# Optimization experiments

Hardware: AMD Instinct MI355X
Metric: run time of the kernel (lower is better)

Reference implementation:

```python
import jax, jax.numpy as jnp
import numpy as np
import math

FEAT, HID, EMB, NCLS = 128, 128, 64, 10
N, E = 50000, 1600000
RATIO = 0.8


def graph_conv(x, src, dst, valid, w_rel, b_rel, w_root):
    # PyG GraphConv: out = lin_rel(sum_{j->i} x_j) + lin_root(x_i)
    msg = jnp.where(valid[:, None], x[src], 0.0)  # [E, C]
    seg = jnp.where(valid, dst, x.shape[0])       # invalid -> dummy bucket
    agg = jax.ops.segment_sum(msg, seg, num_segments=x.shape[0] + 1)[:-1]
    return agg @ w_rel.T + b_rel + x @ w_root.T


def topk_pool(x, src, dst, valid, weight):
    # PyG TopKPooling: score = tanh((x . w) / ||w||); keep top ceil(ratio*N)
    score = jnp.tanh((x @ weight) / jnp.linalg.norm(weight))
    k = int(math.ceil(RATIO * x.shape[0]))
    _, perm = jax.lax.top_k(score, k)
    xp = x[perm] * score[perm][:, None]
    mapping = jnp.full((x.shape[0],), -1, dtype=src.dtype)
    mapping = mapping.at[perm].set(jnp.arange(k, dtype=src.dtype))
    nsrc, ndst = mapping[src], mapping[dst]
    nvalid = valid & (nsrc >= 0) & (ndst >= 0)
    return xp, nsrc, ndst, nvalid, perm


def setup_inputs() -> dict:
    key = jax.random.key(0)
    ks = jax.random.split(key, 24)
    s = 0.05
    inp = {
        'x': jax.random.normal(ks[0], (N, FEAT), dtype=jnp.float32),
        'edge_index': jax.random.randint(ks[1], (2, E), 0, N, dtype=jnp.int32),
        'w1_rel': jax.random.normal(ks[2], (HID, FEAT)) * s,
        'w1_root': jax.random.normal(ks[3], (HID, FEAT)) * s,
        'b1': jnp.zeros((HID,), jnp.float32),
        'p1_w': jax.random.normal(ks[4], (HID,)) * s,
        'w2_rel': jax.random.normal(ks[5], (EMB, HID)) * s,
        'w2_root': jax.random.normal(ks[6], (EMB, HID)) * s,
        'b2': jnp.zeros((EMB,), jnp.float32),
        'p2_w': jax.random.normal(ks[7], (EMB,)) * s,
        'w3_rel': jax.random.normal(ks[8], (EMB, EMB)) * s,
        'w3_root': jax.random.normal(ks[9], (EMB, EMB)) * s,
        'b3': jnp.zeros((EMB,), jnp.float32),
        'w4_rel': jax.random.normal(ks[10], (HID, EMB)) * s,
        'w4_root': jax.random.normal(ks[11], (HID, EMB)) * s,
        'b4': jnp.zeros((HID,), jnp.float32),
        'w5_rel': jax.random.normal(ks[12], (FEAT, HID)) * s,
        'w5_root': jax.random.normal(ks[13], (FEAT, HID)) * s,
        'b5': jnp.zeros((FEAT,), jnp.float32),
        'lin_w': jax.random.normal(ks[14], (NCLS, FEAT)) * s,
        'lin_b': jnp.zeros((NCLS,), jnp.float32),
    }
    return inp


def reference(x, edge_index, w1_rel, w1_root, b1, p1_w, w2_rel, w2_root, b2, p2_w,
              w3_rel, w3_root, b3, w4_rel, w4_root, b4, w5_rel, w5_root, b5,
              lin_w, lin_b):
    src0, dst0 = edge_index[0], edge_index[1]
    valid0 = jnp.ones((src0.shape[0],), dtype=bool)

    x1 = jax.nn.relu(graph_conv(x, src0, dst0, valid0, w1_rel, b1, w1_root))
    xp1, src1, dst1, valid1, perm1 = topk_pool(x1, src0, dst0, valid0, p1_w)
    x2 = jax.nn.relu(graph_conv(xp1, src1, dst1, valid1, w2_rel, b2, w2_root))
    xp2, src2, dst2, valid2, perm2 = topk_pool(x2, src1, dst1, valid1, p2_w)
    x3 = jax.nn.relu(graph_conv(xp2, src2, dst2, valid2, w3_rel, b3, w3_root))
    # Unpool1: scatter x3 into zeros shaped like x2, then skip-add
    u1 = jnp.zeros((x2.shape[0], x3.shape[1]), x3.dtype).at[perm2].set(x3) + x2
    x4 = jax.nn.relu(graph_conv(u1, src1, dst1, valid1, w4_rel, b4, w4_root))
    # Unpool2
    u2 = jnp.zeros((x1.shape[0], x4.shape[1]), x4.dtype).at[perm1].set(x4) + x1
    x5 = jax.nn.relu(graph_conv(u2, src0, dst0, valid0, w5_rel, b5, w5_root))
    return jax.nn.log_softmax(x5 @ lin_w.T + lin_b, axis=-1)
```

## Files before the change

### kernel.cpp

```cpp
#include <hip/hip_runtime.h>
#include <hip/hip_bf16.h>
#include <math.h>

#define N0 50000
#define E0 1600000
#define K1 40000
#define K2 32000
#define FEAT 128
#define HID 128
#define EMB 64
#define NCLS 10

#define RADIX_BINS 4096

#define NB 391
#define PB_CH 8192
#define BCAP 5120

#define SCHUNK 2048

typedef __bf16 v8bf __attribute__((ext_vector_type(8)));
typedef __bf16 v4bf __attribute__((ext_vector_type(4)));
typedef float  v4f  __attribute__((ext_vector_type(4)));
typedef unsigned short u16;

static __device__ __forceinline__ unsigned f2key(float f) {
    unsigned u = __float_as_uint(f);
    return (u & 0x80000000u) ? ~u : (u | 0x80000000u);
}

struct SelCtl { unsigned long long prefix; int kRem; int counter; };

__global__ void detect_dtype_kernel(const unsigned* __restrict__ w, int n, int* __restrict__ flag) {
    __shared__ int tot;
    if (threadIdx.x == 0) tot = 0;
    __syncthreads();
    int cnt = 0;
    for (int i = threadIdx.x; i < n; i += 256) {
        unsigned lo = w[i] & 0xFFFFu;
        unsigned e = (lo >> 7) & 0xFFu;
        cnt += (e >= 143);
    }
    atomicAdd(&tot, cnt);
    __syncthreads();
    if (threadIdx.x == 0) flag[0] = (tot > n / 8) ? 1 : 0;
}

static __device__ __forceinline__ float load_as_f32(const void* in, long long i, int isF32) {
    if (isF32) return ((const float*)in)[i];
    unsigned short h = ((const unsigned short*)in)[i];
    return __uint_as_float(((unsigned)h) << 16);
}

__global__ void x_convert_kernel(const void* __restrict__ in, float* __restrict__ xf,
                                 __bf16* __restrict__ hi, __bf16* __restrict__ lo, int n,
                                 const int* __restrict__ flag) {
    int i = blockIdx.x * 256 + threadIdx.x;
    if (i >= n) return;
    float v = load_as_f32(in, i, *flag);
    __bf16 h = (__bf16)v;
    int row = i >> 7, c = i & 127;
    xf[(((size_t)(c >> 4)) * N0 + row) * 16 + (c & 15)] = v;
    hi[i] = h; lo[i] = (__bf16)(v - (float)h);
}

struct SplitJob { const void* src; __bf16* hi; __bf16* lo; int n; };
struct SplitJobs { SplitJob j[10]; };
__global__ void split_all_kernel(SplitJobs jobs, const int* __restrict__ flag) {
    SplitJob jb = jobs.j[blockIdx.y];
    int i = blockIdx.x * 256 + threadIdx.x;
    if (i >= jb.n) return;
    float v = load_as_f32(jb.src, i, *flag);
    __bf16 h = (__bf16)v;
    jb.hi[i] = h; jb.lo[i] = (__bf16)(v - (float)h);
}

struct F32Job { const void* src; float* dst; int n; };
struct F32Jobs { F32Job j[9]; };
__global__ void f32_all_kernel(F32Jobs jobs, const int* __restrict__ flag) {
    F32Job jb = jobs.j[blockIdx.x];
    for (int i = threadIdx.x; i < jb.n; i += 256) jb.dst[i] = load_as_f32(jb.src, i, *flag);
}

template<int KEYS>
__global__ void lookback_scan_kernel(const int* __restrict__ deg,
                                     const unsigned long long* __restrict__ keys,
                                     const SelCtl* __restrict__ ctl, int M,
                                     int* __restrict__ flags,
                                     int* __restrict__ rowp,
                                     int* __restrict__ perm,
                                     int* __restrict__ mapping) {
    int b = blockIdx.x;
    int t = threadIdx.x;
    int lane = t & 63, wave = t >> 6;
    int idx = b * SCHUNK + t * 8;
    unsigned long long thr = KEYS ? ctl->prefix : 0ull;
    int v[8];
#pragma unroll
    for (int k = 0; k < 8; ++k) {
        int j = idx + k;
        if (KEYS) v[k] = (j < M) ? (int)(keys[j] >= thr) : 0;
        else      v[k] = (j < M) ? deg[j] : 0;
    }
    int s = 0;
#pragma unroll
    for (int k = 0; k < 8; ++k) { int tmp = v[k]; v[k] = s; s += tmp; }
    int incl = s;
    for (int off = 1; off < 64; off <<= 1) {
        int u = __shfl_up(incl, off, 64);
        if (lane >= off) incl += u;
    }
    int texcl = incl - s;
    __shared__ int ws[4];
    __shared__ int pfxs;
    if (lane == 63) ws[wave] = incl;
    __syncthreads();
    int woff = 0, T = 0;
    for (int w = 0; w < 4; ++w) { if (w < wave) woff += ws[w]; T += ws[w]; }
    if (t == 0) {
        __threadfence();
        atomicExch(&flags[b], T + 1);
        int sum = 0;
        for (int p = 0; p < b; ++p) {
            int f;
            while ((f = atomicAdd(&flags[p], 0)) == 0) { }
            sum += f - 1;
        }
        pfxs = sum;
    }
    __syncthreads();
    int off0 = pfxs + woff + texcl;
    if (!KEYS) {
#pragma unroll
        for (int k = 0; k < 8; ++k) {
            int j = idx + k;
            if (j < M) rowp[j] = off0 + v[k];
        }
        if (b == gridDim.x - 1 && t == 255) rowp[M] = pfxs + T;
    } else {
#pragma unroll
        for (int k = 0; k < 8; ++k) {
            int j = idx + k;
            if (j < M) {
                if (keys[j] >= thr) { int r = off0 + v[k]; perm[r] = j; mapping[j] = r; }
                else mapping[j] = -1;
            }
        }
    }
}

__global__ void bucket_count_kernel(const int* __restrict__ dst, int E, int* __restrict__ bktCnt) {
    __shared__ int cnt[NB];
    for (int b = threadIdx.x; b < NB; b += 256) cnt[b] = 0;
    __syncthreads();
    int e = blockIdx.x * PB_CH;
    int e1 = E < e + PB_CH ? E : e + PB_CH;
    for (int i = e + threadIdx.x; i < e1; i += 256)
        atomicAdd(&cnt[dst[i] >> 7], 1);
    __syncthreads();
    for (int b = threadIdx.x; b < NB; b += 256) {
        int c = cnt[b];
        if (c) atomicAdd(&bktCnt[b], c);
    }
}

__global__ void scan_nb_kernel(const int* __restrict__ bktCnt, int* __restrict__ bktBase,
                               int* __restrict__ bcur, int* __restrict__ rpM, int E) {
    __shared__ int sc[512];
    int t = threadIdx.x;
    int v = (t < NB) ? bktCnt[t] : 0;
    sc[t] = v;
    __syncthreads();
    for (int off = 1; off < 512; off <<= 1) {
        int u = 0;
        if (t >= off) u = sc[t - off];
        __syncthreads();
        if (t >= off) sc[t] += u;
        __syncthreads();
    }
    if (t < NB) {
        int base = sc[t] - v;
        bktBase[t] = base;
        bcur[t] = base;
    }
    if (t == 0) { bktBase[NB] = E; rpM[0] = E; }
}

__global__ void edge_partition_kernel(const int* __restrict__ src, const int* __restrict__ dst, int E,
                                      int* __restrict__ bcur, unsigned* __restrict__ pairBuf) {
    __shared__ int cnt[NB];
    __shared__ int bas[NB];
    for (int b = threadIdx.x; b < NB; b += 256) cnt[b] = 0;
    __syncthreads();
    int e0 = blockIdx.x * PB_CH;
    int e1 = E < e0 + PB_CH ? E : e0 + PB_CH;
    for (int e = e0 + threadIdx.x; e < e1; e += 256)
        atomicAdd(&cnt[dst[e] >> 7], 1);
    __syncthreads();
    for (int b = threadIdx.x; b < NB; b += 256) {
        int c = cnt[b];
        bas[b] = c ? atomicAdd(&bcur[b], c) : 0;
        cnt[b] = 0;
    }
    __syncthreads();
    for (int e = e0 + threadIdx.x; e < e1; e += 256) {
        int s = src[e];
        int d = dst[e];
        int b = d >> 7;
        int r = atomicAdd(&cnt[b], 1);
        unsigned pv = ((unsigned)(d & 127) << 16) | (unsigned)s;
        __builtin_nontemporal_store(pv, pairBuf + bas[b] + r);
    }
}

__global__ void bucket_fill_kernel(const unsigned* __restrict__ pairBuf, const int* __restrict__ bktBase,
                                   int Mrows, u16* __restrict__ cols, int* __restrict__ rowptr) {
    int b = blockIdx.x;
    int d0 = b << 7;
    int d1 = d0 + 128; if (d1 > Mrows) d1 = Mrows;
    int segBase = bktBase[b], segEnd = bktBase[b + 1];
    int size = segEnd - segBase;
    int tid = threadIdx.x;
    __shared__ int cnt[128];
    __shared__ int sc[128];
    __shared__ int cur[128];
    __shared__ u16 stage[BCAP];
    if (tid < 128) cnt[tid] = 0;
    __syncthreads();
    for (int t = tid; t < size; t += 256)
        atomicAdd(&cnt[pairBuf[segBase + t] >> 16], 1);
    __syncthreads();
    if (tid < 128) sc[tid] = cnt[tid];
    __syncthreads();
    for (int off = 1; off < 128; off <<= 1) {
        int u = 0;
        if (tid < 128 && tid >= off) u = sc[tid - off];
        __syncthreads();
        if (tid < 128 && tid >= off) sc[tid] += u;
        __syncthreads();
    }
    if (tid < 128) {
        int excl = sc[tid] - cnt[tid];
        cur[tid] = excl;
        if (d0 + tid < d1) rowptr[d0 + tid] = segBase + excl;
    }
    __syncthreads();
    if (size <= BCAP) {
        for (int t = tid; t < size; t += 256) {
            unsigned p = pairBuf[segBase + t];
            int pos = atomicAdd(&cur[p >> 16], 1);
            stage[pos] = (u16)(p & 0xFFFFu);
        }
        __syncthreads();
        for (int t = tid; t < size; t += 256)
            __builtin_nontemporal_store(stage[t], cols + segBase + t);
    } else {
        for (int t = tid; t < size; t += 256) {
            unsigned p = pairBuf[segBase + t];
            int pos = atomicAdd(&cur[p >> 16], 1);
            cols[segBase + pos] = (u16)(p & 0xFFFFu);
        }
    }
}

__global__ void deg_filter_kernel(const int* __restrict__ rowptr, const u16* __restrict__ cols,
                                  const int* __restrict__ map, int Mold, int* __restrict__ deg) {
    int d = blockIdx.x * 256 + threadIdx.x;
    if (d >= Mold) return;
    int nd = map[d];
    if (nd < 0) return;
    int b = rowptr[d], e = rowptr[d + 1];
    int c = 0;
    for (int j = b; j < e; ++j) c += (map[cols[j]] >= 0);
    deg[nd] = c;
}

__global__ void csr_filter_fill_kernel(const int* __restrict__ rowptr, const u16* __restrict__ cols,
                                       const int* __restrict__ map, int Mold,
                                       const int* __restrict__ newrp, u16* __restrict__ ncols) {
    int d = blockIdx.x * 256 + threadIdx.x;
    if (d >= Mold) return;
    int nd = map[d];
    if (nd < 0) return;
    int w = newrp[nd];
    int b = rowptr[d], e = rowptr[d + 1];
    for (int j = b; j < e; ++j) {
        int ns = map[cols[j]];
        if (ns >= 0) ncols[w++] = (u16)ns;
    }
}

template<int C>
__global__ void __launch_bounds__(256, 8)
aggregate_kernel(const int* __restrict__ rowptr, const u16* __restrict__ cols,
                 const float* __restrict__ xs, __bf16* __restrict__ aggHi,
                 __bf16* __restrict__ aggLo, int M) {
    const int SW = C / 8;
    const int LPR = SW / 4;
    const int RPB = 256 / LPR;
    int sl = blockIdx.x & 7;
    int n  = (blockIdx.x >> 3) * RPB + threadIdx.x / LPR;
    int c4 = threadIdx.x % LPR;
    if (n >= M) return;
    const float* xsl = xs + (size_t)sl * M * SW + (size_t)c4 * 4;
    int b = rowptr[n], e = rowptr[n + 1];
    float4 s = {0.f, 0.f, 0.f, 0.f};
    int j = b;
    for (; j + 8 <= e; j += 8) {
        int i0 = cols[j],     i1 = cols[j + 1], i2 = cols[j + 2], i3 = cols[j + 3];
        int i4 = cols[j + 4], i5 = cols[j + 5], i6 = cols[j + 6], i7 = cols[j + 7];
        float4 v0 = *(const float4*)(xsl + (size_t)i0 * SW);
        float4 v1 = *(const float4*)(xsl + (size_t)i1 * SW);
        float4 v2 = *(const float4*)(xsl + (size_t)i2 * SW);
        float4 v3 = *(const float4*)(xsl + (size_t)i3 * SW);
        float4 v4 = *(const float4*)(xsl + (size_t)i4 * SW);
        float4 v5 = *(const float4*)(xsl + (size_t)i5 * SW);
        float4 v6 = *(const float4*)(xsl + (size_t)i6 * SW);
        float4 v7 = *(const float4*)(xsl + (size_t)i7 * SW);
        s.x += v0.x; s.y += v0.y; s.z += v0.z; s.w += v0.w;
        s.x += v1.x; s.y += v1.y; s.z += v1.z; s.w += v1.w;
        s.x += v2.x; s.y += v2.y; s.z += v2.z; s.w += v2.w;
        s.x += v3.x; s.y += v3.y; s.z += v3.z; s.w += v3.w;
        s.x += v4.x; s.y += v4.y; s.z += v4.z; s.w += v4.w;
        s.x += v5.x; s.y += v5.y; s.z += v5.z; s.w += v5.w;
        s.x += v6.x; s.y += v6.y; s.z += v6.z; s.w += v6.w;
        s.x += v7.x; s.y += v7.y; s.z += v7.z; s.w += v7.w;
    }
    for (; j < e; ++j) {
        int i0 = cols[j];
        float4 v0 = *(const float4*)(xsl + (size_t)i0 * SW);
        s.x += v0.x; s.y += v0.y; s.z += v0.z; s.w += v0.w;
    }
    v4bf h, l;
    h[0] = (__bf16)s.x; l[0] = (__bf16)(s.x - (float)h[0]);
    h[1] = (__bf16)s.y; l[1] = (__bf16)(s.y - (float)h[1]);
    h[2] = (__bf16)s.z; l[2] = (__bf16)(s.z - (float)h[2]);
    h[3] = (__bf16)s.w; l[3] = (__bf16)(s.w - (float)h[3]);
    size_t o = ((size_t)sl * M + n) * SW + c4 * 4;
    __builtin_nontemporal_store(h, (v4bf*)(aggHi + o));
    __builtin_nontemporal_store(l, (v4bf*)(aggLo + o));
}

template<int Cin, int Cout, bool SCORE>
__global__ void __launch_bounds__(256, 8)
linear_mfma_kernel(int M,
                   const __bf16* __restrict__ Ahi, const __bf16* __restrict__ Alo,
                   const __bf16* __restrict__ WaHi, const __bf16* __restrict__ WaLo,
                   const __bf16* __restrict__ Bhi, const __bf16* __restrict__ Blo,
                   const __bf16* __restrict__ WbHi, const __bf16* __restrict__ WbLo,
                   const float* __restrict__ bias, float* __restrict__ outF,
                   const float* __restrict__ sw, float* __restrict__ score,
                   unsigned long long* __restrict__ keys) {
    constexpr int NG = Cout / 32;
    constexpr int SW2 = Cin / 8;
    int wave = threadIdx.x >> 6;
    int lane = threadIdx.x & 63;
    int m = lane & 15, quad = lane >> 4;
    int r16  = wave & 1;
    int colh = wave >> 1;
    int row0 = blockIdx.x * 32 + r16 * 16;
    int ra = row0 + m; if (ra > M - 1) ra = M - 1;
    int cbase = colh * (Cout / 2);

    v4f acc[NG];
#pragma unroll
    for (int g = 0; g < NG; ++g) acc[g] = (v4f){0.f, 0.f, 0.f, 0.f};

#pragma unroll
    for (int ks = 0; ks < Cin / 32; ++ks) {
        int col0 = ks * 32 + quad * 8;
        int sl = col0 / SW2, off = col0 % SW2;
        size_t aoff = ((size_t)sl * M + ra) * SW2 + off;
        v8bf ah = *(const v8bf*)(Ahi + aoff);
        v8bf al = *(const v8bf*)(Alo + aoff);
#pragma unroll
        for (int g = 0; g < NG; ++g) {
            size_t woff = (size_t)(cbase + g * 16 + m) * Cin + ks * 32 + quad * 8;
            v8bf bh = *(const v8bf*)(WaHi + woff);
            v8bf bl = *(const v8bf*)(WaLo + woff);
            acc[g] = __builtin_amdgcn_mfma_f32_16x16x32_bf16(ah, bh, acc[g], 0, 0, 0);
            acc[g] = __builtin_amdgcn_mfma_f32_16x16x32_bf16(ah, bl, acc[g], 0, 0, 0);
            acc[g] = __builtin_amdgcn_mfma_f32_16x16x32_bf16(al, bh, acc[g], 0, 0, 0);
        }
    }
#pragma unroll
    for (int ks = 0; ks < Cin / 32; ++ks) {
        size_t aoff = (size_t)ra * Cin + ks * 32 + quad * 8;
        v8bf ah = *(const v8bf*)(Bhi + aoff);
        v8bf al = *(const v8bf*)(Blo + aoff);
#pragma unroll
        for (int g = 0; g < NG; ++g) {
            size_t woff = (size_t)(cbase + g * 16 + m) * Cin + ks * 32 + quad * 8;
            v8bf bh = *(const v8bf*)(WbHi + woff);
            v8bf bl = *(const v8bf*)(WbLo + woff);
            acc[g] = __builtin_amdgcn_mfma_f32_16x16x32_bf16(ah, bh, acc[g], 0, 0, 0);
            acc[g] = __builtin_amdgcn_mfma_f32_16x16x32_bf16(ah, bl, acc[g], 0, 0, 0);
            acc[g] = __builtin_amdgcn_mfma_f32_16x16x32_bf16(al, bh, acc[g], 0, 0, 0);
        }
    }

#pragma unroll
    for (int g = 0; g < NG; ++g) {
        int col = cbase + g * 16 + m;
        float bv = bias[col];
#pragma unroll
        for (int r = 0; r < 4; ++r) {
            int row = row0 + quad * 4 + r;
            if (row < M) outF[(size_t)row * Cout + col] = fmaxf(acc[g][r] + bv, 0.f);
        }
    }

    if (SCORE) {
        __shared__ float pl[2][32];
        float wv[NG];
#pragma unroll
        for (int g = 0; g < NG; ++g) wv[g] = sw[cbase + g * 16 + m];
#pragma unroll
        for (int r = 0; r < 4; ++r) {
            float p = 0.f;
#pragma unroll
            for (int g = 0; g < NG; ++g) {
                float ov = fmaxf(acc[g][r] + bias[cbase + g * 16 + m], 0.f);
                p += ov * wv[g];
            }
#pragma unroll
            for (int off = 1; off < 16; off <<= 1) p += __shfl_xor(p, off, 64);
            if (m == 0) pl[colh][r16 * 16 + quad * 4 + r] = p;
        }
        __syncthreads();
        if (threadIdx.x < 32) {
            int row = blockIdx.x * 32 + threadIdx.x;
            if (row < M) {
                float p = pl[0][threadIdx.x] + pl[1][threadIdx.x];
                float q = 0.f;
                for (int c = 0; c < Cout; ++c) { float w = sw[c]; q += w * w; }
                float sc = (float)tanh((double)(p / sqrtf(q)));
                score[row] = sc;
                keys[row] = ((unsigned long long)f2key(sc) << 16) |
                            (unsigned long long)(0xFFFFu ^ (unsigned)row);
            }
        }
    }
}

__global__ void radix_hist_kernel(const unsigned long long* __restrict__ keys, int N,
                                  int* __restrict__ hist, const SelCtl* __restrict__ ctl, int pass) {
    __shared__ int lh[RADIX_BINS];
    for (int b = threadIdx.x; b < RADIX_BINS; b += 256) lh[b] = 0;
    __syncthreads();
    int shift = 36 - 12 * pass;
    unsigned long long pref = (pass > 0) ? ctl->prefix : 0ull;
    for (int i = blockIdx.x * 256 + threadIdx.x; i < N; i += gridDim.x * 256) {
        unsigned long long key = keys[i];
        if (pass > 0 && (key >> (shift + 12)) != pref) continue;
        atomicAdd(&lh[(int)((key >> shift) & 0xFFFull)], 1);
    }
    __syncthreads();
    for (int b = threadIdx.x; b < RADIX_BINS; b += 256) {
        int c = lh[b];
        if (c) atomicAdd(&hist[b], c);
    }
}

__global__ void radix_select_kernel(int* __restrict__ hist, SelCtl* __restrict__ ctl,
                                    int K, int pass) {
    __shared__ int wtot[16];
    int t = threadIdx.x;
    int lane = t & 63, wave = t >> 6;
    int kRem = (pass == 0) ? K : ctl->kRem;
    unsigned long long oldPrefix = (pass == 0) ? 0ull : ctl->prefix;
    int base = t * 4;
    int h0 = hist[base], h1 = hist[base + 1], h2 = hist[base + 2], h3 = hist[base + 3];
    int tot = h0 + h1 + h2 + h3;
    int incl = tot;
#pragma unroll
    for (int off = 1; off < 64; off <<= 1) {
        int u = __shfl_down(incl, off, 64);
        if (lane + off < 64) incl += u;
    }
    if (lane == 0) wtot[wave] = incl;
    __syncthreads();
    int wsuf = 0;
#pragma unroll
    for (int w = 0; w < 16; ++w) if (w > wave) wsuf += wtot[w];
    int sExcl = wsuf + (incl - tot);
    if (sExcl < kRem && kRem <= sExcl + tot) {
        int c = sExcl;
        int hv[4] = {h0, h1, h2, h3};
        for (int k = 3; k >= 0; --k) {
            int h = hv[k];
            if (c + h >= kRem) {
                ctl->prefix = (oldPrefix << 12) | (unsigned long long)(base + k);
                ctl->kRem = kRem - c;
                ctl->counter = 0;
                break;
            }
            c += h;
        }
    }
    hist[base] = 0; hist[base + 1] = 0; hist[base + 2] = 0; hist[base + 3] = 0;
}

template<int C>
__global__ void pool_apply_kernel(const float* __restrict__ xin, const float* __restrict__ score,
                                  const int* __restrict__ perm, float* __restrict__ xpF,
                                  __bf16* __restrict__ xpHi, __bf16* __restrict__ xpLo, int K) {
    const int CH = C / 4;
    const int SW = C / 8;
    int tid = blockIdx.x * 256 + threadIdx.x;
    int j = tid / CH, c4 = tid % CH;
    if (j >= K) return;
    int src = perm[j];
    float s = score[src];
    float4 v = ((const float4*)(xin + (size_t)src * C))[c4];
    v.x *= s; v.y *= s; v.z *= s; v.w *= s;
    int sl = (c4 * 4) / SW, off = (c4 * 4) % SW;
    *(float4*)(xpF + ((size_t)sl * K + j) * SW + off) = v;
    v4bf h, l;
    h[0] = (__bf16)v.x; l[0] = (__bf16)(v.x - (float)h[0]);
    h[1] = (__bf16)v.y; l[1] = (__bf16)(v.y - (float)h[1]);
    h[2] = (__bf16)v.z; l[2] = (__bf16)(v.z - (float)h[2]);
    h[3] = (__bf16)v.w; l[3] = (__bf16)(v.w - (float)h[3]);
    *(v4bf*)(xpHi + (size_t)j * C + c4 * 4) = h;
    *(v4bf*)(xpLo + (size_t)j * C + c4 * 4) = l;
}

template<int C>
__global__ void unpool_add_kernel(const float* __restrict__ base, const float* __restrict__ deep,
                                  const int* __restrict__ mapping, float* __restrict__ uF,
                                  __bf16* __restrict__ uHi, __bf16* __restrict__ uLo, int M) {
    const int CH = C / 4;
    const int SW = C / 8;
    int tid = blockIdx.x * 256 + threadIdx.x;
    int j = tid / CH, c4 = tid % CH;
    if (j >= M) return;
    float4 v = ((const float4*)(base + (size_t)j * C))[c4];
    int m = mapping[j];
    if (m >= 0) {
        float4 d = ((const float4*)(deep + (size_t)m * C))[c4];
        v.x += d.x; v.y += d.y; v.z += d.z; v.w += d.w;
    }
    int sl = (c4 * 4) / SW, off = (c4 * 4) % SW;
    *(float4*)(uF + ((size_t)sl * M + j) * SW + off) = v;
    v4bf h, l;
    h[0] = (__bf16)v.x; l[0] = (__bf16)(v.x - (float)h[0]);
    h[1] = (__bf16)v.y; l[1] = (__bf16)(v.y - (float)h[1]);
    h[2] = (__bf16)v.z; l[2] = (__bf16)(v.z - (float)h[2]);
    h[3] = (__bf16)v.w; l[3] = (__bf16)(v.w - (float)h[3]);
    *(v4bf*)(uHi + (size_t)j * C + c4 * 4) = h;
    *(v4bf*)(uLo + (size_t)j * C + c4 * 4) = l;
}

__global__ void head_kernel(const float* __restrict__ x5, const float* __restrict__ lw,
                            const float* __restrict__ lb, void* __restrict__ out, int M,
                            const int* __restrict__ flag) {
    int row = blockIdx.x * 4 + (threadIdx.x >> 6);
    int lane = threadIdx.x & 63;
    if (row >= M) return;
    float a0 = x5[(size_t)row * 128 + lane];
    float a1 = x5[(size_t)row * 128 + 64 + lane];
    float d[NCLS];
#pragma unroll
    for (int o = 0; o < NCLS; ++o) {
        float p = a0 * lw[o * 128 + lane] + a1 * lw[o * 128 + 64 + lane];
#pragma unroll
        for (int off = 32; off >= 1; off >>= 1) p += __shfl_xor(p, off, 64);
        d[o] = p + lb[o];
    }
    float mx = d[0];
#pragma unroll
    for (int o = 1; o < NCLS; ++o) mx = fmaxf(mx, d[o]);
    float s = 0.f;
#pragma unroll
    for (int o = 0; o < NCLS; ++o) s += expf(d[o] - mx);
    float lse = mx + logf(s);
    if (lane < NCLS) {
        float v = d[0];
#pragma unroll
        for (int o = 1; o < NCLS; ++o) if (lane == o) v = d[o];
        float r = v - lse;
        if (*flag) ((float*)out)[(size_t)row * NCLS + lane] = r;
        else ((__hip_bfloat16*)out)[(size_t)row * NCLS + lane] = __float2bfloat16(r);
    }
}

extern "C" void kernel_launch(void* const* d_in, const int* in_sizes, int n_in,
                              void* d_out, int out_size, void* d_ws, size_t ws_size,
                              hipStream_t stream) {
    const void* x_raw   = d_in[0];
    const int*  ei      = (const int*)d_in[1];
    const void* w1_rel  = d_in[2];
    const void* w1_root = d_in[3];
    const void* b1      = d_in[4];
    const void* p1w     = d_in[5];
    const void* w2_rel  = d_in[6];
    const void* w2_root = d_in[7];
    const void* b2      = d_in[8];
    const void* p2w     = d_in[9];
    const void* w3_rel  = d_in[10];
    const void* w3_root = d_in[11];
    const void* b3      = d_in[12];
    const void* w4_rel  = d_in[13];
    const void* w4_root = d_in[14];
    const void* b4      = d_in[15];
    const void* w5_rel  = d_in[16];
    const void* w5_root = d_in[17];
    const void* b5      = d_in[18];
    const void* lw      = d_in[19];
    const void* lb      = d_in[20];

    char* base = (char*)d_ws;
    size_t off = 0;
    auto alloc = [&](size_t bytes) -> void* {
        void* p = base + off;
        off = (off + bytes + 255) & ~(size_t)255;
        return p;
    };
    int* flag = (int*)alloc(256);
    __bf16* w1rHi = (__bf16*)alloc(HID * FEAT * 2); __bf16* w1rLo = (__bf16*)alloc(HID * FEAT * 2);
    __bf16* w1tHi = (__bf16*)alloc(HID * FEAT * 2); __bf16* w1tLo = (__bf16*)alloc(HID * FEAT * 2);
    __bf16* w2rHi = (__bf16*)alloc(EMB * HID * 2);  __bf16* w2rLo = (__bf16*)alloc(EMB * HID * 2);
    __bf16* w2tHi = (__bf16*)alloc(EMB * HID * 2);  __bf16* w2tLo = (__bf16*)alloc(EMB * HID * 2);
    __bf16* w3rHi = (__bf16*)alloc(EMB * EMB * 2);  __bf16* w3rLo = (__bf16*)alloc(EMB * EMB * 2);
    __bf16* w3tHi = (__bf16*)alloc(EMB * EMB * 2);  __bf16* w3tLo = (__bf16*)alloc(EMB * EMB * 2);
    __bf16* w4rHi = (__bf16*)alloc(HID * EMB * 2);  __bf16* w4rLo = (__bf16*)alloc(HID * EMB * 2);
    __bf16* w4tHi = (__bf16*)alloc(HID * EMB * 2);  __bf16* w4tLo = (__bf16*)alloc(HID * EMB * 2);
    __bf16* w5rHi = (__bf16*)alloc(FEAT * HID * 2); __bf16* w5rLo = (__bf16*)alloc(FEAT * HID * 2);
    __bf16* w5tHi = (__bf16*)alloc(FEAT * HID * 2); __bf16* w5tLo = (__bf16*)alloc(FEAT * HID * 2);
    float* b1f = (float*)alloc(HID * 4);
    float* b2f = (float*)alloc(EMB * 4);
    float* b3f = (float*)alloc(EMB * 4);
    float* b4f = (float*)alloc(HID * 4);
    float* b5f = (float*)alloc(FEAT * 4);
    float* p1f = (float*)alloc(HID * 4);
    float* p2f = (float*)alloc(EMB * 4);
    float* lwf = (float*)alloc(NCLS * FEAT * 4);
    float* lbf = (float*)alloc(NCLS * 4);
    float* score = (float*)alloc((size_t)N0 * 4);
    unsigned long long* keys = (unsigned long long*)alloc((size_t)N0 * 8);
    char* zeroArena = (char*)alloc(RADIX_BINS * 4 + 2048 + 1024);
    int* hist    = (int*)zeroArena;
    int* bktCnt  = (int*)(zeroArena + RADIX_BINS * 4);
    int* flags0  = (int*)(zeroArena + RADIX_BINS * 4 + 2048);
    int* flags1  = flags0 + 64;
    int* flags2  = flags0 + 128;
    int* flags3  = flags0 + 192;
    SelCtl* ctl = (SelCtl*)alloc(256);
    int* perm1 = (int*)alloc((size_t)K1 * 4);
    int* map1  = (int*)alloc((size_t)N0 * 4);
    int* perm2 = (int*)alloc((size_t)K2 * 4);
    int* map2  = (int*)alloc((size_t)K1 * 4);
    int* deg   = (int*)alloc((size_t)(N0 + 1) * 4);
    int* rp0   = (int*)alloc((size_t)(N0 + 1) * 4);
    int* rp1   = (int*)alloc((size_t)(K1 + 1) * 4);
    int* rp2   = (int*)alloc((size_t)(K2 + 1) * 4);
    int* bktBase= (int*)alloc((size_t)(NB + 1) * 4);
    int* bcur  = (int*)alloc((size_t)NB * 4);
    u16* cols0 = (u16*)alloc((size_t)E0 * 2);
    u16* cols1 = (u16*)alloc((size_t)E0 * 2);
    u16* cols2 = (u16*)alloc((size_t)E0 * 2);
    char* ubuf = (char*)alloc((size_t)K1 * 64 * 4 + (size_t)N0 * 128 * 4);
    unsigned* pairBuf = (unsigned*)ubuf;
    float* u1s = (float*)ubuf;
    float* u2s = (float*)(ubuf + (size_t)K1 * 64 * 4);
    char*   arenaX  = (char*)alloc((size_t)N0 * 128 * 4);
    __bf16* arenaHi = (__bf16*)alloc((size_t)N0 * 128 * 2);
    __bf16* arenaLo = (__bf16*)alloc((size_t)N0 * 128 * 2);
    __bf16* aggHi   = (__bf16*)alloc((size_t)N0 * 128 * 2);
    __bf16* aggLo   = (__bf16*)alloc((size_t)N0 * 128 * 2);
    float*  x1f     = (float*)alloc((size_t)N0 * 128 * 4);
    float*  x2f     = (float*)alloc((size_t)K1 * 64 * 4);

    float* xf   = (float*)arenaX;
    float* xp1f = (float*)arenaX;
    float* xp2f = (float*)arenaX;
    float* x3f  = (float*)(arenaX + 8388608);
    float* x4f  = (float*)arenaX;
    float* x5f  = (float*)arenaX;
    __bf16 *xHi = arenaHi,  *xLo = arenaLo;
    __bf16 *xp1Hi = arenaHi, *xp1Lo = arenaLo;
    __bf16 *xp2Hi = arenaHi, *xp2Lo = arenaLo;
    __bf16 *u1Hi = arenaHi,  *u1Lo = arenaLo;
    __bf16 *u2Hi = arenaHi,  *u2Lo = arenaLo;

    const int* src0 = ei;
    const int* dst0 = ei + E0;

    auto g = [](long long n, int b) -> unsigned { return (unsigned)((n + b - 1) / b); };

    detect_dtype_kernel<<<1, 256, 0, stream>>>((const unsigned*)x_raw, 4096, flag);
    hipMemsetAsync(zeroArena, 0, RADIX_BINS * 4 + 2048 + 1024, stream);
    x_convert_kernel<<<g((long long)N0 * FEAT, 256), 256, 0, stream>>>(x_raw, xf, xHi, xLo, N0 * FEAT, flag);
    {
        SplitJobs sj;
        sj.j[0] = {w1_rel,  w1rHi, w1rLo, HID * FEAT};
        sj.j[1] = {w1_root, w1tHi, w1tLo, HID * FEAT};
        sj.j[2] = {w2_rel,  w2rHi, w2rLo, EMB * HID};
        sj.j[3] = {w2_root, w2tHi, w2tLo, EMB * HID};
        sj.j[4] = {w3_rel,  w3rHi, w3rLo, EMB * EMB};
        sj.j[5] = {w3_root, w3tHi, w3tLo, EMB * EMB};
        sj.j[6] = {w4_rel,  w4rHi, w4rLo, HID * EMB};
        sj.j[7] = {w4_root, w4tHi, w4tLo, HID * EMB};
        sj.j[8] = {w5_rel,  w5rHi, w5rLo, FEAT * HID};
        sj.j[9] = {w5_root, w5tHi, w5tLo, FEAT * HID};
        dim3 grid(g(HID * FEAT, 256), 10);
        split_all_kernel<<<grid, 256, 0, stream>>>(sj, flag);
    }
    {
        F32Jobs fj;
        fj.j[0] = {b1, b1f, HID};
        fj.j[1] = {b2, b2f, EMB};
        fj.j[2] = {b3, b3f, EMB};
        fj.j[3] = {b4, b4f, HID};
        fj.j[4] = {b5, b5f, FEAT};
        fj.j[5] = {p1w, p1f, HID};
        fj.j[6] = {p2w, p2f, EMB};
        fj.j[7] = {lw, lwf, NCLS * FEAT};
        fj.j[8] = {lb, lbf, NCLS};
        f32_all_kernel<<<9, 256, 0, stream>>>(fj, flag);
    }

    bucket_count_kernel<<<g(E0, PB_CH), 256, 0, stream>>>(dst0, E0, bktCnt);
    scan_nb_kernel<<<1, 512, 0, stream>>>(bktCnt, bktBase, bcur, rp0 + N0, E0);
    edge_partition_kernel<<<g(E0, PB_CH), 256, 0, stream>>>(src0, dst0, E0, bcur, pairBuf);
    bucket_fill_kernel<<<NB, 256, 0, stream>>>(pairBuf, bktBase, N0, cols0, rp0);

    aggregate_kernel<128><<<g(N0, 64) * 8, 256, 0, stream>>>(rp0, cols0, xf, aggHi, aggLo, N0);
    linear_mfma_kernel<128, 128, true><<<g(N0, 32), 256, 0, stream>>>(N0, aggHi, aggLo, w1rHi, w1rLo,
                                                                      xHi, xLo, w1tHi, w1tLo, b1f, x1f,
                                                                      p1f, score, keys);

    for (int pass = 0; pass < 4; ++pass) {
        radix_hist_kernel<<<64, 256, 0, stream>>>(keys, N0, hist, ctl, pass);
        radix_select_kernel<<<1, 1024, 0, stream>>>(hist, ctl, K1, pass);
    }
    lookback_scan_kernel<1><<<g(N0, SCHUNK), 256, 0, stream>>>(nullptr, keys, ctl, N0, flags0,
                                                               nullptr, perm1, map1);
    pool_apply_kernel<128><<<g((long long)K1 * 32, 256), 256, 0, stream>>>(x1f, score, perm1, xp1f, xp1Hi, xp1Lo, K1);

    deg_filter_kernel<<<g(N0, 256), 256, 0, stream>>>(rp0, cols0, map1, N0, deg);
    lookback_scan_kernel<0><<<g(K1, SCHUNK), 256, 0, stream>>>(deg, nullptr, nullptr, K1, flags1,
                                                               rp1, nullptr, nullptr);
    csr_filter_fill_kernel<<<g(N0, 256), 256, 0, stream>>>(rp0, cols0, map1, N0, rp1, cols1);

    aggregate_kernel<128><<<g(K1, 64) * 8, 256, 0, stream>>>(rp1, cols1, xp1f, aggHi, aggLo, K1);
    linear_mfma_kernel<128, 64, true><<<g(K1, 32), 256, 0, stream>>>(K1, aggHi, aggLo, w2rHi, w2rLo,
                                                                     xp1Hi, xp1Lo, w2tHi, w2tLo, b2f, x2f,
                                                                     p2f, score, keys);

    for (int pass = 0; pass < 4; ++pass) {
        radix_hist_kernel<<<64, 256, 0, stream>>>(keys, K1, hist, ctl, pass);
        radix_select_kernel<<<1, 1024, 0, stream>>>(hist, ctl, K2, pass);
    }
    lookback_scan_kernel<1><<<g(K1, SCHUNK), 256, 0, stream>>>(nullptr, keys, ctl, K1, flags2,
                                                               nullptr, perm2, map2);
    pool_apply_kernel<64><<<g((long long)K2 * 16, 256), 256, 0, stream>>>(x2f, score, perm2, xp2f, xp2Hi, xp2Lo, K2);

    deg_filter_kernel<<<g(K1, 256), 256, 0, stream>>>(rp1, cols1, map2, K1, deg);
    lookback_scan_kernel<0><<<g(K2, SCHUNK), 256, 0, stream>>>(deg, nullptr, nullptr, K2, flags3,
                                                               rp2, nullptr, nullptr);
    csr_filter_fill_kernel<<<g(K1, 256), 256, 0, stream>>>(rp1, cols1, map2, K1, rp2, cols2);

    aggregate_kernel<64><<<g(K2, 128) * 8, 256, 0, stream>>>(rp2, cols2, xp2f, aggHi, aggLo, K2);
    linear_mfma_kernel<64, 64, false><<<g(K2, 32), 256, 0, stream>>>(K2, aggHi, aggLo, w3rHi, w3rLo,
                                                                     xp2Hi, xp2Lo, w3tHi, w3tLo, b3f, x3f,
                                                                     nullptr, nullptr, nullptr);

    unpool_add_kernel<64><<<g((long long)K1 * 16, 256), 256, 0, stream>>>(x2f, x3f, map2, u1s, u1Hi, u1Lo, K1);

    aggregate_kernel<64><<<g(K1, 128) * 8, 256, 0, stream>>>(rp1, cols1, u1s, aggHi, aggLo, K1);
    linear_mfma_kernel<64, 128, false><<<g(K1, 32), 256, 0, stream>>>(K1, aggHi, aggLo, w4rHi, w4rLo,
                                                                      u1Hi, u1Lo, w4tHi, w4tLo, b4f, x4f,
                                                                      nullptr, nullptr, nullptr);

    unpool_add_kernel<128><<<g((long long)N0 * 32, 256), 256, 0, stream>>>(x1f, x4f, map1, u2s, u2Hi, u2Lo, N0);

    aggregate_kernel<128><<<g(N0, 64) * 8, 256, 0, stream>>>(rp0, cols0, u2s, aggHi, aggLo, N0);
    linear_mfma_kernel<128, 128, false><<<g(N0, 32), 256, 0, stream>>>(N0, aggHi, aggLo, w5rHi, w5rLo,
                                                                       u2Hi, u2Lo, w5tHi, w5tLo, b5f, x5f,
                                                                       nullptr, nullptr, nullptr);

    head_kernel<<<g(N0, 4), 256, 0, stream>>>(x5f, lwf, lbf, d_out, N0, flag);
}
```

Baseline: 885.5 us.

## Fuse radix top-k select passes and compaction into one persistent grid-barrier kernel

Replaces the eight radix histogram/select launches plus the lookback-scan compaction per pooling stage with a single 64-block persistent kernel. The blocks synchronize through a global atomic grid barrier and block 0 performs each select step. This removes about eighteen small kernel launches and their launch gaps. It relies on all 64 blocks being co-resident for the spin barrier, and the final compaction walks each thread's contiguous chunk serially.

```diff
diff --git a/kernel.cpp b/kernel.cpp
--- a/kernel.cpp
+++ b/kernel.cpp
@@ -146,6 +146,115 @@
                 else mapping[j] = -1;
             }
         }
+    }
+}
+
+__global__ void __launch_bounds__(256)
+radix_pool_kernel(const unsigned long long* __restrict__ keys, int N, int K,
+                  int* __restrict__ hist, SelCtl* __restrict__ ctl,
+                  int* __restrict__ gbar, int* __restrict__ btot,
+                  int* __restrict__ perm, int* __restrict__ mapping) {
+    int b = blockIdx.x, t = threadIdx.x;
+    int lane = t & 63, wave = t >> 6;
+    __shared__ int lh[RADIX_BINS];
+    __shared__ int wsh[4];
+    __shared__ int bpfx;
+    int gen = 0;
+    auto gridbar = [&]() {
+        __threadfence();
+        __syncthreads();
+        ++gen;
+        if (t == 0) {
+            atomicAdd(gbar, 1);
+            while (atomicAdd(gbar, 0) < gen * 64) { }
+        }
+        __syncthreads();
+    };
+
+    unsigned long long prefix = 0;
+    int kRem = K;
+    for (int pass = 0; pass < 4; ++pass) {
+        for (int i = t; i < RADIX_BINS; i += 256) lh[i] = 0;
+        __syncthreads();
+        int shift = 36 - 12 * pass;
+        for (int i = b * 256 + t; i < N; i += 64 * 256) {
+            unsigned long long key = keys[i];
+            if (pass > 0 && (key >> (shift + 12)) != prefix) continue;
+            atomicAdd(&lh[(int)((key >> shift) & 0xFFFull)], 1);
+        }
+        __syncthreads();
+        for (int i = t; i < RADIX_BINS; i += 256) {
+            int c = lh[i];
+            if (c) atomicAdd(&hist[i], c);
+        }
+        gridbar();
+        if (b == 0) {
+            int base = t * 16;
+            int hv[16]; int tot = 0;
+#pragma unroll
+            for (int k = 0; k < 16; ++k) { hv[k] = atomicAdd(&hist[base + k], 0); tot += hv[k]; }
+            int incl = tot;
+#pragma unroll
+            for (int off = 1; off < 64; off <<= 1) {
+                int u = __shfl_down(incl, off, 64);
+                if (lane + off < 64) incl += u;
+            }
+            if (lane == 0) wsh[wave] = incl;
+            __syncthreads();
+            int wsuf = 0;
+            for (int w = wave + 1; w < 4; ++w) wsuf += wsh[w];
+            int sExcl = wsuf + (incl - tot);
+            if (sExcl < kRem && kRem <= sExcl + tot) {
+                int c = sExcl;
+                for (int k = 15; k >= 0; --k) {
+                    int h = hv[k];
+                    if (c + h >= kRem) {
+                        atomicExch((unsigned long long*)&ctl->prefix,
+                                   (prefix << 12) | (unsigned long long)(base + k));
+                        atomicExch(&ctl->kRem, kRem - c);
+                        break;
+                    }
+                    c += h;
+                }
+            }
+#pragma unroll
+            for (int k = 0; k < 16; ++k) atomicExch(&hist[base + k], 0);
+        }
+        gridbar();
+        prefix = atomicAdd((unsigned long long*)&ctl->prefix, 0ull);
+        kRem = atomicAdd(&ctl->kRem, 0);
+    }
+
+    int CH = (N + 63) >> 6;
+    int ECH = (CH + 255) >> 8;
+    int lim = b * CH + CH; if (lim > N) lim = N;
+    int i0 = b * CH + t * ECH; if (i0 > lim) i0 = lim;
+    int i1 = i0 + ECH; if (i1 > lim) i1 = lim;
+    int cnt = 0;
+    for (int i = i0; i < i1; ++i) cnt += (keys[i] >= prefix);
+    int incl = cnt;
+    for (int off = 1; off < 64; off <<= 1) {
+        int u = __shfl_up(incl, off, 64);
+        if (lane >= off) incl += u;
+    }
+    int texcl = incl - cnt;
+    __syncthreads();
+    if (lane == 63) wsh[wave] = incl;
+    __syncthreads();
+    int woff = 0, T = 0;
+    for (int w = 0; w < 4; ++w) { if (w < wave) woff += wsh[w]; T += wsh[w]; }
+    if (t == 0) atomicExch(&btot[b], T);
+    gridbar();
+    if (t == 0) {
+        int sum = 0;
+        for (int p = 0; p < b; ++p) sum += atomicAdd(&btot[p], 0);
+        bpfx = sum;
+    }
+    __syncthreads();
+    int r = bpfx + woff + texcl;
+    for (int i = i0; i < i1; ++i) {
+        if (keys[i] >= prefix) { perm[r] = i; mapping[i] = r; ++r; }
+        else mapping[i] = -1;
     }
 }
 
@@ -443,64 +552,6 @@
     }
 }
 
-__global__ void radix_hist_kernel(const unsigned long long* __restrict__ keys, int N,
-                                  int* __restrict__ hist, const SelCtl* __restrict__ ctl, int pass) {
-    __shared__ int lh[RADIX_BINS];
-    for (int b = threadIdx.x; b < RADIX_BINS; b += 256) lh[b] = 0;
-    __syncthreads();
-    int shift = 36 - 12 * pass;
-    unsigned long long pref = (pass > 0) ? ctl->prefix : 0ull;
-    for (int i = blockIdx.x * 256 + threadIdx.x; i < N; i += gridDim.x * 256) {
-        unsigned long long key = keys[i];
-        if (pass > 0 && (key >> (shift + 12)) != pref) continue;
-        atomicAdd(&lh[(int)((key >> shift) & 0xFFFull)], 1);
-    }
-    __syncthreads();
-    for (int b = threadIdx.x; b < RADIX_BINS; b += 256) {
-        int c = lh[b];
-        if (c) atomicAdd(&hist[b], c);
-    }
-}
-
-__global__ void radix_select_kernel(int* __restrict__ hist, SelCtl* __restrict__ ctl,
-                                    int K, int pass) {
-    __shared__ int wtot[16];
-    int t = threadIdx.x;
-    int lane = t & 63, wave = t >> 6;
-    int kRem = (pass == 0) ? K : ctl->kRem;
-    unsigned long long oldPrefix = (pass == 0) ? 0ull : ctl->prefix;
-    int base = t * 4;
-    int h0 = hist[base], h1 = hist[base + 1], h2 = hist[base + 2], h3 = hist[base + 3];
-    int tot = h0 + h1 + h2 + h3;
-    int incl = tot;
-#pragma unroll
-    for (int off = 1; off < 64; off <<= 1) {
-        int u = __shfl_down(incl, off, 64);
-        if (lane + off < 64) incl += u;
-    }
-    if (lane == 0) wtot[wave] = incl;
-    __syncthreads();
-    int wsuf = 0;
-#pragma unroll
-    for (int w = 0; w < 16; ++w) if (w > wave) wsuf += wtot[w];
-    int sExcl = wsuf + (incl - tot);
-    if (sExcl < kRem && kRem <= sExcl + tot) {
-        int c = sExcl;
-        int hv[4] = {h0, h1, h2, h3};
-        for (int k = 3; k >= 0; --k) {
-            int h = hv[k];
-            if (c + h >= kRem) {
-                ctl->prefix = (oldPrefix << 12) | (unsigned long long)(base + k);
-                ctl->kRem = kRem - c;
-                ctl->counter = 0;
-                break;
-            }
-            c += h;
-        }
-    }
-    hist[base] = 0; hist[base + 1] = 0; hist[base + 2] = 0; hist[base + 3] = 0;
-}
-
 template<int C>
 __global__ void pool_apply_kernel(const float* __restrict__ xin, const float* __restrict__ score,
                                   const int* __restrict__ perm, float* __restrict__ xpF,
@@ -638,14 +689,15 @@
     float* lbf = (float*)alloc(NCLS * 4);
     float* score = (float*)alloc((size_t)N0 * 4);
     unsigned long long* keys = (unsigned long long*)alloc((size_t)N0 * 8);
-    char* zeroArena = (char*)alloc(RADIX_BINS * 4 + 2048 + 1024);
+    char* zeroArena = (char*)alloc(RADIX_BINS * 4 + 2048 + 512 + 512);
     int* hist    = (int*)zeroArena;
     int* bktCnt  = (int*)(zeroArena + RADIX_BINS * 4);
-    int* flags0  = (int*)(zeroArena + RADIX_BINS * 4 + 2048);
-    int* flags1  = flags0 + 64;
-    int* flags2  = flags0 + 128;
-    int* flags3  = flags0 + 192;
+    int* flags1  = (int*)(zeroArena + RADIX_BINS * 4 + 2048);
+    int* flags3  = flags1 + 64;
+    int* gbar1   = (int*)(zeroArena + RADIX_BINS * 4 + 2048 + 512);
+    int* gbar2   = gbar1 + 64;
     SelCtl* ctl = (SelCtl*)alloc(256);
+    int* btot  = (int*)alloc(64 * 4);
     int* perm1 = (int*)alloc((size_t)K1 * 4);
     int* map1  = (int*)alloc((size_t)N0 * 4);
     int* perm2 = (int*)alloc((size_t)K2 * 4);
@@ -689,7 +741,7 @@
     auto g = [](long long n, int b) -> unsigned { return (unsigned)((n + b - 1) / b); };
 
     detect_dtype_kernel<<<1, 256, 0, stream>>>((const unsigned*)x_raw, 4096, flag);
-    hipMemsetAsync(zeroArena, 0, RADIX_BINS * 4 + 2048 + 1024, stream);
+    hipMemsetAsync(zeroArena, 0, RADIX_BINS * 4 + 2048 + 512 + 512, stream);
     x_convert_kernel<<<g((long long)N0 * FEAT, 256), 256, 0, stream>>>(x_raw, xf, xHi, xLo, N0 * FEAT, flag);
     {
         SplitJobs sj;
@@ -730,12 +782,7 @@
                                                                       xHi, xLo, w1tHi, w1tLo, b1f, x1f,
                                                                       p1f, score, keys);
 
-    for (int pass = 0; pass < 4; ++pass) {
-        radix_hist_kernel<<<64, 256, 0, stream>>>(keys, N0, hist, ctl, pass);
-        radix_select_kernel<<<1, 1024, 0, stream>>>(hist, ctl, K1, pass);
-    }
-    lookback_scan_kernel<1><<<g(N0, SCHUNK), 256, 0, stream>>>(nullptr, keys, ctl, N0, flags0,
-                                                               nullptr, perm1, map1);
+    radix_pool_kernel<<<64, 256, 0, stream>>>(keys, N0, K1, hist, ctl, gbar1, btot, perm1, map1);
     pool_apply_kernel<128><<<g((long long)K1 * 32, 256), 256, 0, stream>>>(x1f, score, perm1, xp1f, xp1Hi, xp1Lo, K1);
 
     deg_filter_kernel<<<g(N0, 256), 256, 0, stream>>>(rp0, cols0, map1, N0, deg);
@@ -748,12 +795,7 @@
                                                                      xp1Hi, xp1Lo, w2tHi, w2tLo, b2f, x2f,
                                                                      p2f, score, keys);
 
-    for (int pass = 0; pass < 4; ++pass) {
-        radix_hist_kernel<<<64, 256, 0, stream>>>(keys, K1, hist, ctl, pass);
-        radix_select_kernel<<<1, 1024, 0, stream>>>(hist, ctl, K2, pass);
-    }
-    lookback_scan_kernel<1><<<g(K1, SCHUNK), 256, 0, stream>>>(nullptr, keys, ctl, K1, flags2,
-                                                               nullptr, perm2, map2);
+    radix_pool_kernel<<<64, 256, 0, stream>>>(keys, K1, K2, hist, ctl, gbar2, btot, perm2, map2);
     pool_apply_kernel<64><<<g((long long)K2 * 16, 256), 256, 0, stream>>>(x2f, score, perm2, xp2f, xp2Hi, xp2Lo, K2);
 
     deg_filter_kernel<<<g(K1, 256), 256, 0, stream>>>(rp1, cols1, map2, K1, deg);
```

After: 984.4 us. 1.11x slower.
